# Performance work log

Measured on AMD Instinct MI355X. Metric: run time of the kernel, lower is better.

Reference implementation:

```python
import jax, jax.numpy as jnp
import numpy as np

S, B, E, H = 2048, 2, 1024, 16
D = E // H  # head_dim = 64


def setup_inputs() -> dict:
    key = jax.random.key(0)
    ks = jax.random.split(key, 11)
    std = 1.0 / np.sqrt(E)
    return {
        "query": jax.random.normal(ks[0], (S, B, E), jnp.float32),
        "key": jax.random.normal(ks[1], (S, B, E), jnp.float32),
        "value": jax.random.normal(ks[2], (S, B, E), jnp.float32),
        "q_w": jax.random.uniform(ks[3], (E, E), jnp.float32, -std, std),
        "q_b": jax.random.uniform(ks[4], (E,), jnp.float32, -std, std),
        "k_w": jax.random.uniform(ks[5], (E, E), jnp.float32, -std, std),
        "k_b": jax.random.uniform(ks[6], (E,), jnp.float32, -std, std),
        "v_w": jax.random.uniform(ks[7], (E, E), jnp.float32, -std, std),
        "v_b": jax.random.uniform(ks[8], (E,), jnp.float32, -std, std),
        "out_w": jax.random.uniform(ks[9], (E, E), jnp.float32, -std, std),
        "out_b": jax.random.uniform(ks[10], (E,), jnp.float32, -std, std),
    }


def reference(query, key, value, q_w, q_b, k_w, k_b, v_w, v_b, out_w, out_b):
    tgt_len, bsz, embed_dim = query.shape
    src_len = key.shape[0]
    head_dim = embed_dim // H
    scaling = head_dim ** -0.5

    # nn.Linear: x @ W.T + b
    q = (jnp.einsum('sbe,fe->sbf', query, q_w) + q_b) * scaling
    k = jnp.einsum('sbe,fe->sbf', key, k_w) + k_b
    v = jnp.einsum('sbe,fe->sbf', value, v_w) + v_b

    # [S, B, E] -> [B*H, S, D]
    def split_heads(x, n):
        return x.reshape(n, bsz * H, head_dim).transpose(1, 0, 2)

    q = split_heads(q, tgt_len)
    k = split_heads(k, src_len)
    v = split_heads(v, src_len)

    scores = jnp.einsum('bqd,bkd->bqk', q, k)        # [B*H, S, S]
    attn = jax.nn.softmax(scores, axis=-1)            # dropout p=0 -> identity
    out = jnp.einsum('bqk,bkd->bqd', attn, v)         # [B*H, S, D]
    out = out.transpose(1, 0, 2).reshape(tgt_len, bsz, embed_dim)
    Z = jnp.einsum('sbe,fe->sbf', out, out_w) + out_b
    attn_avg = attn.reshape(bsz, H, tgt_len, src_len).sum(axis=1) / H
    return Z, attn_avg
```

## Files before the change

kernel.cpp:

```cpp
#include <hip/hip_runtime.h>
#include <hip/hip_fp16.h>
#include <cstdint>
#include <cstddef>

#define S_LEN 2048
#define BATCH 2
#define EMB   1024
#define NHEAD 16
#define HDIM  64

typedef short short8 __attribute__((ext_vector_type(8)));
typedef float f32x4  __attribute__((ext_vector_type(4)));

__device__ __forceinline__ unsigned short f2b(float f) {
    unsigned int u = __float_as_uint(f);
    u = (u + 0x7FFFu + ((u >> 16) & 1u)) >> 16;
    return (unsigned short)u;
}
__device__ __forceinline__ unsigned int pk2(float a, float b) {
    return (unsigned int)f2b(a) | ((unsigned int)f2b(b) << 16);
}
__device__ __forceinline__ float b2f_lo(unsigned int u) { return __uint_as_float(u << 16); }
__device__ __forceinline__ float b2f_hi(unsigned int u) { return __uint_as_float(u & 0xFFFF0000u); }

__device__ __forceinline__ void gload_lds16(const ushort* g, ushort* l) {
    __builtin_amdgcn_global_load_lds(
        (const __attribute__((address_space(1))) void*)g,
        (__attribute__((address_space(3))) void*)l, 16, 0, 0);
}

__global__ __launch_bounds__(256)
void cast3(const float* __restrict__ s0, const float* __restrict__ s1,
           const float* __restrict__ s2, ushort* __restrict__ d0,
           ushort* __restrict__ d1, ushort* __restrict__ d2)
{
    const float* s = (blockIdx.y == 0) ? s0 : (blockIdx.y == 1) ? s1 : s2;
    ushort*      d = (blockIdx.y == 0) ? d0 : (blockIdx.y == 1) ? d1 : d2;
    const size_t i = ((size_t)blockIdx.x * 256 + threadIdx.x) * 8;
    const float4 a = *(const float4*)(s + i);
    const float4 b = *(const float4*)(s + i + 4);
    *(uint4*)(d + i) = make_uint4(pk2(a.x, a.y), pk2(a.z, a.w),
                                  pk2(b.x, b.y), pk2(b.z, b.w));
}

__global__ __launch_bounds__(256)
void cast4(const float* __restrict__ s0, const float* __restrict__ s1,
           const float* __restrict__ s2, const float* __restrict__ s3,
           ushort* __restrict__ d0, ushort* __restrict__ d1,
           ushort* __restrict__ d2, ushort* __restrict__ d3)
{
    const float* s = (blockIdx.y == 0) ? s0 : (blockIdx.y == 1) ? s1
                   : (blockIdx.y == 2) ? s2 : s3;
    ushort*      d = (blockIdx.y == 0) ? d0 : (blockIdx.y == 1) ? d1
                   : (blockIdx.y == 2) ? d2 : d3;
    const size_t i = ((size_t)blockIdx.x * 256 + threadIdx.x) * 8;
    const float4 a = *(const float4*)(s + i);
    const float4 b = *(const float4*)(s + i + 4);
    *(uint4*)(d + i) = make_uint4(pk2(a.x, a.y), pk2(a.z, a.w),
                                  pk2(b.x, b.y), pk2(b.z, b.w));
}

__device__ __forceinline__ void gemm_core(
    ushort (*As)[128 * 32], ushort (*Bs)[128 * 32],
    const ushort* __restrict__ A, const ushort* __restrict__ W,
    const float* __restrict__ bias, void* __restrict__ out_,
    float scale, int mode)
{
    constexpr int K  = EMB;
    constexpr int NT = K / 32;

    const int t    = threadIdx.x;
    const int lane = t & 63;
    const int wave = t >> 6;
    const int quad = lane >> 4;
    const int l15  = lane & 15;
    const int wm   = wave >> 2;
    const int wn   = wave & 3;
    const int m0   = blockIdx.x * 128;
    const int n0   = blockIdx.y * 128;

    const int srow = t >> 2;
    const int sseg = ((t & 3) ^ ((srow >> 1) & 3)) << 3;
    const ushort* gA = A + (size_t)(m0 + srow) * K + sseg;
    const ushort* gW = W + (size_t)(n0 + srow) * K + sseg;

    f32x4 acc[4][2];
#pragma unroll
    for (int mi = 0; mi < 4; ++mi)
#pragma unroll
        for (int ni = 0; ni < 2; ++ni) acc[mi][ni] = (f32x4){0.f, 0.f, 0.f, 0.f};

#define STAGE(buf, kt) do {                         \
        gload_lds16(gA + (kt) * 32, &As[buf][t * 8]); \
        gload_lds16(gW + (kt) * 32, &Bs[buf][t * 8]); \
    } while (0)

    STAGE(0, 0);
    __syncthreads();

    for (int kt = 0; kt < NT; ++kt) {
        const int cur = kt & 1;
        if (kt + 1 < NT) STAGE(cur ^ 1, kt + 1);
        short8 af[4], bf[2];
#pragma unroll
        for (int mi = 0; mi < 4; ++mi) {
            const int ra = wm * 64 + mi * 16 + l15;
            af[mi] = *(const short8*)&As[cur][ra * 32 + ((quad ^ ((ra >> 1) & 3)) << 3)];
        }
#pragma unroll
        for (int ni = 0; ni < 2; ++ni) {
            const int rb = wn * 32 + ni * 16 + l15;
            bf[ni] = *(const short8*)&Bs[cur][rb * 32 + ((quad ^ ((rb >> 1) & 3)) << 3)];
        }
#pragma unroll
        for (int mi = 0; mi < 4; ++mi)
#pragma unroll
            for (int ni = 0; ni < 2; ++ni)
                acc[mi][ni] = __builtin_amdgcn_mfma_f32_16x16x32_bf16(
                    af[mi], bf[ni], acc[mi][ni], 0, 0, 0);
        __syncthreads();
    }
#undef STAGE

#pragma unroll
    for (int mi = 0; mi < 4; ++mi)
#pragma unroll
        for (int ni = 0; ni < 2; ++ni) {
            const int col = n0 + wn * 32 + ni * 16 + l15;
            const float bc = bias[col];
#pragma unroll
            for (int r = 0; r < 4; ++r) {
                const int rg = m0 + wm * 64 + mi * 16 + quad * 4 + r;
                const float v = (acc[mi][ni][r] + bc) * scale;
                if (mode == 0) {
                    ((float*)out_)[(size_t)rg * EMB + col] = v;
                } else {
                    const int s  = rg >> 1;
                    const int bb = rg & 1;
                    const int h  = col >> 6;
                    const int d  = col & 63;
                    if (mode == 1)
                        ((ushort*)out_)[(((size_t)(bb * NHEAD + h)) * S_LEN + s) * HDIM + d] = f2b(v);
                    else
                        ((ushort*)out_)[(((size_t)(bb * NHEAD + h)) * HDIM + d) * S_LEN + s] = f2b(v);
                }
            }
        }
}

__global__ __launch_bounds__(512, 2)
void gemm_qkv(const ushort* __restrict__ qi, const ushort* __restrict__ ki,
              const ushort* __restrict__ vi,
              const ushort* __restrict__ qW, const ushort* __restrict__ kW,
              const ushort* __restrict__ vW,
              const float* __restrict__ qB, const float* __restrict__ kB,
              const float* __restrict__ vB,
              ushort* __restrict__ qO, ushort* __restrict__ kO,
              ushort* __restrict__ vO)
{
    __shared__ ushort As[2][128 * 32];
    __shared__ ushort Bs[2][128 * 32];
    const int z = blockIdx.z;
    const ushort* A    = (z == 0) ? qi : (z == 1) ? ki : vi;
    const ushort* W    = (z == 0) ? qW : (z == 1) ? kW : vW;
    const float* bias  = (z == 0) ? qB : (z == 1) ? kB : vB;
    ushort* out        = (z == 0) ? qO : (z == 1) ? kO : vO;
    const float scale  = (z == 0) ? 0.125f : 1.0f;
    const int   mode   = (z == 2) ? 2 : 1;
    gemm_core(As, Bs, A, W, bias, out, scale, mode);
}

__global__ __launch_bounds__(512, 2)
void gemm_z(const ushort* __restrict__ A, const ushort* __restrict__ W,
            const float* __restrict__ bias, float* __restrict__ out)
{
    __shared__ ushort As[2][128 * 32];
    __shared__ ushort Bs[2][128 * 32];
    gemm_core(As, Bs, A, W, bias, out, 1.0f, 0);
}

#define PLD 2056
__global__ __launch_bounds__(512, 4)
void attn_bf16(const ushort* __restrict__ qw, const ushort* __restrict__ kw,
               const ushort* __restrict__ vt, ushort* __restrict__ ao,
               float* __restrict__ rinv_ws)
{
    __shared__ ushort pLds[16 * PLD];
    __shared__ float  redS[8 * 16];
    __shared__ float  red2[4 * 16 * 16];

    const int t     = threadIdx.x;
    const int lane  = t & 63;
    const int wave  = t >> 6;
    const int quad  = lane >> 4;
    const int l15   = lane & 15;
    const int rbase = quad * 4;

    const int bid     = blockIdx.x;
    const int logical = (bid & 7) * 64 + (bid >> 3);
    const int qt      = logical & 127;
    const int rest    = logical >> 7;
    const int b       = rest & 1;
    const int g       = rest >> 1;
    const int sq0     = qt * 16;

    const int ntile = wave & 3;
    const int khalf = wave >> 2;

    for (int hh = 0; hh < 8; ++hh) {
        const int h  = g * 8 + hh;
        const int bh = b * NHEAD + h;
        const ushort* qbase = qw + ((size_t)bh * S_LEN + sq0) * HDIM;
        const ushort* kbse  = kw + (size_t)bh * S_LEN * HDIM;

        const short8 qf0 = *(const short8*)(qbase + l15 * HDIM + quad * 8);
        const short8 qf1 = *(const short8*)(qbase + l15 * HDIM + 32 + quad * 8);

        float s4[4] = {0.f, 0.f, 0.f, 0.f};
#pragma unroll
        for (int ti = 0; ti < 16; ++ti) {
            const int c0 = wave * 256 + ti * 16;
            const ushort* kr = kbse + (size_t)(c0 + l15) * HDIM;
            const short8 k0 = *(const short8*)(kr + quad * 8);
            const short8 k1 = *(const short8*)(kr + 32 + quad * 8);
            f32x4 a = (f32x4){0.f, 0.f, 0.f, 0.f};
            a = __builtin_amdgcn_mfma_f32_16x16x32_bf16(qf0, k0, a, 0, 0, 0);
            a = __builtin_amdgcn_mfma_f32_16x16x32_bf16(qf1, k1, a, 0, 0, 0);
#pragma unroll
            for (int r = 0; r < 4; ++r) {
                const float e = exp2f(fmaf(a[r], 1.44269504f, -11.54156035f));
                s4[r] += e;
                pLds[(rbase + r) * PLD + c0 + l15] = f2b(e);
            }
        }
#pragma unroll
        for (int off = 1; off < 16; off <<= 1)
#pragma unroll
            for (int r = 0; r < 4; ++r) s4[r] += __shfl_xor(s4[r], off, 16);
        if (l15 == 0)
#pragma unroll
            for (int r = 0; r < 4; ++r) redS[wave * 16 + rbase + r] = s4[r];
        __syncthreads();

        float rinv[4];
#pragma unroll
        for (int r = 0; r < 4; ++r) {
            float s = redS[rbase + r];
#pragma unroll
            for (int w = 1; w < 8; ++w) s += redS[w * 16 + rbase + r];
            rinv[r] = 1.0f / s;
        }
        if (wave == 0 && l15 == 0) {
#pragma unroll
            for (int r = 0; r < 4; ++r)
                rinv_ws[(size_t)bh * S_LEN + sq0 + rbase + r] = rinv[r];
        }

        const ushort* vrow = vt + ((size_t)bh * HDIM + ntile * 16 + l15) * S_LEN + khalf * 1024;
        const ushort* prow = &pLds[l15 * PLD + khalf * 1024];
        f32x4 o0 = (f32x4){0.f, 0.f, 0.f, 0.f}, o1 = o0;
#pragma unroll
        for (int st = 0; st < 32; st += 2) {
            const short8 pa0 = *(const short8*)(prow + st * 32 + quad * 8);
            const short8 vb0 = *(const short8*)(vrow + st * 32 + quad * 8);
            o0 = __builtin_amdgcn_mfma_f32_16x16x32_bf16(pa0, vb0, o0, 0, 0, 0);
            const short8 pa1 = *(const short8*)(prow + (st + 1) * 32 + quad * 8);
            const short8 vb1 = *(const short8*)(vrow + (st + 1) * 32 + quad * 8);
            o1 = __builtin_amdgcn_mfma_f32_16x16x32_bf16(pa1, vb1, o1, 0, 0, 0);
        }
        const f32x4 o = o0 + o1;
        if (khalf == 1) {
#pragma unroll
            for (int r = 0; r < 4; ++r)
                red2[ntile * 256 + (rbase + r) * 16 + l15] = o[r];
        }
        __syncthreads();
        if (khalf == 0) {
#pragma unroll
            for (int r = 0; r < 4; ++r) {
                const float val = (o[r] + red2[ntile * 256 + (rbase + r) * 16 + l15]) * rinv[r];
                const int s = sq0 + rbase + r;
                const int d = ntile * 16 + l15;
                ao[((size_t)s * BATCH + b) * EMB + h * HDIM + d] = f2b(val);
            }
        }
    }
}

__global__ __launch_bounds__(512, 2)
void pavg_scores(const ushort* __restrict__ qw, const ushort* __restrict__ kw,
                 const float* __restrict__ rinv_ws, float* __restrict__ out)
{
    const int t     = threadIdx.x;
    const int lane  = t & 63;
    const int wave  = t >> 6;
    const int quad  = lane >> 4;
    const int l15   = lane & 15;
    const int rbase = quad * 4;

    const int bid     = blockIdx.x;
    const int logical = (bid & 7) * 64 + (bid >> 3);
    const int kc      = logical >> 6;
    const int b       = (logical >> 5) & 1;
    const int sqc     = logical & 31;

    const int k0row = kc * 256 + wave * 32;

    float pacc[4][2][4];
#pragma unroll
    for (int s4i = 0; s4i < 4; ++s4i)
#pragma unroll
        for (int t2 = 0; t2 < 2; ++t2)
#pragma unroll
            for (int r = 0; r < 4; ++r) pacc[s4i][t2][r] = 0.f;

    for (int h = 0; h < NHEAD; ++h) {
        const int bh = b * NHEAD + h;
        const ushort* kr0 = kw + ((size_t)bh * S_LEN + k0row + l15) * HDIM;
        const ushort* kr1 = kw + ((size_t)bh * S_LEN + k0row + 16 + l15) * HDIM;
        const short8 kf00 = *(const short8*)(kr0 + quad * 8);
        const short8 kf01 = *(const short8*)(kr0 + 32 + quad * 8);
        const short8 kf10 = *(const short8*)(kr1 + quad * 8);
        const short8 kf11 = *(const short8*)(kr1 + 32 + quad * 8);
        const float* rbse = rinv_ws + (size_t)bh * S_LEN + sqc * 64;
#pragma unroll
        for (int s4i = 0; s4i < 4; ++s4i) {
            const ushort* qbase = qw + ((size_t)bh * S_LEN + sqc * 64 + s4i * 16) * HDIM;
            const short8 qf0 = *(const short8*)(qbase + l15 * HDIM + quad * 8);
            const short8 qf1 = *(const short8*)(qbase + l15 * HDIM + 32 + quad * 8);
            f32x4 a0 = (f32x4){0.f, 0.f, 0.f, 0.f}, a1 = a0;
            a0 = __builtin_amdgcn_mfma_f32_16x16x32_bf16(qf0, kf00, a0, 0, 0, 0);
            a0 = __builtin_amdgcn_mfma_f32_16x16x32_bf16(qf1, kf01, a0, 0, 0, 0);
            a1 = __builtin_amdgcn_mfma_f32_16x16x32_bf16(qf0, kf10, a1, 0, 0, 0);
            a1 = __builtin_amdgcn_mfma_f32_16x16x32_bf16(qf1, kf11, a1, 0, 0, 0);
#pragma unroll
            for (int r = 0; r < 4; ++r) {
                const float ri = rbse[s4i * 16 + rbase + r];
                pacc[s4i][0][r] = fmaf(exp2f(fmaf(a0[r], 1.44269504f, -11.54156035f)), ri, pacc[s4i][0][r]);
                pacc[s4i][1][r] = fmaf(exp2f(fmaf(a1[r], 1.44269504f, -11.54156035f)), ri, pacc[s4i][1][r]);
            }
        }
    }

    const float inv16 = 0.0625f;
#pragma unroll
    for (int s4i = 0; s4i < 4; ++s4i)
#pragma unroll
        for (int t2 = 0; t2 < 2; ++t2)
#pragma unroll
            for (int r = 0; r < 4; ++r) {
                const int sq = sqc * 64 + s4i * 16 + rbase + r;
                const int sk = k0row + t2 * 16 + l15;
                out[((size_t)b * S_LEN + sq) * S_LEN + sk] = pacc[s4i][t2][r] * inv16;
            }
}

extern "C" void kernel_launch(void* const* d_in, const int* in_sizes, int n_in,
                              void* d_out, int out_size, void* d_ws, size_t ws_size,
                              hipStream_t stream)
{
    const float* query = (const float*)d_in[0];
    const float* key   = (const float*)d_in[1];
    const float* value = (const float*)d_in[2];
    const float* q_w   = (const float*)d_in[3];
    const float* q_b   = (const float*)d_in[4];
    const float* k_w   = (const float*)d_in[5];
    const float* k_b   = (const float*)d_in[6];
    const float* v_w   = (const float*)d_in[7];
    const float* v_b   = (const float*)d_in[8];
    const float* out_w = (const float*)d_in[9];
    const float* out_b = (const float*)d_in[10];

    float* Z        = (float*)d_out;
    float* attn_avg = Z + (size_t)S_LEN * BATCH * EMB;

    const size_t QKV = (size_t)S_LEN * BATCH * EMB;
    ushort* q_ws    = (ushort*)d_ws;
    ushort* k_ws    = q_ws + QKV;
    ushort* vt_ws   = k_ws + QKV;
    ushort* ao_ws   = vt_ws + QKV;
    float*  rinv_ws = (float*)(ao_ws + QKV);
    ushort* qbf     = (ushort*)(rinv_ws + (size_t)BATCH * NHEAD * S_LEN);
    ushort* kbf     = qbf + QKV;
    ushort* vbf     = kbf + QKV;
    ushort* wqb     = vbf + QKV;
    ushort* wkb     = wqb + (size_t)EMB * EMB;
    ushort* wvb     = wkb + (size_t)EMB * EMB;
    ushort* wob     = wvb + (size_t)EMB * EMB;

    cast3<<<dim3(2048, 3), 256, 0, stream>>>(query, key, value, qbf, kbf, vbf);
    cast4<<<dim3(512, 4), 256, 0, stream>>>(q_w, k_w, v_w, out_w, wqb, wkb, wvb, wob);

    const dim3 blkG(512);
    const dim3 gq(32, 8, 3);
    gemm_qkv<<<gq, blkG, 0, stream>>>(qbf, kbf, vbf, wqb, wkb, wvb,
                                      q_b, k_b, v_b, q_ws, k_ws, vt_ws);

    attn_bf16<<<dim3(512), dim3(512), 0, stream>>>(q_ws, k_ws, vt_ws, ao_ws, rinv_ws);

    const dim3 gz(32, 8);
    gemm_z<<<gz, blkG, 0, stream>>>(ao_ws, wob, out_b, Z);

    pavg_scores<<<dim3(512), dim3(512), 0, stream>>>(q_ws, k_ws, rinv_ws, attn_avg);
}
```

Before: 518.1 us.

## Double-buffer K tiles in LDS and cache row inverses in pavg_scores

The head-averaged score kernel now stages each head's 256x64 K tile into LDS through async global-to-LDS loads, using an XOR swizzle and two buffers so the load for the next head overlaps compute on the current one. It also preloads all 16 heads' softmax row inverses for the block's 64 query rows into shared memory once. This replaces per-wave direct global K fragment loads and repeated global reads of the inverses. In exchange it uses about 68 KB of LDS per block and adds a barrier per head, which may cut occupancy against the launch bound of 2 blocks.

```diff
diff --git a/kernel.cpp b/kernel.cpp
--- a/kernel.cpp
+++ b/kernel.cpp
@@ -291,6 +291,9 @@
 void pavg_scores(const ushort* __restrict__ qw, const ushort* __restrict__ kw,
                  const float* __restrict__ rinv_ws, float* __restrict__ out)
 {
+    __shared__ ushort Kb[2][256 * 64];
+    __shared__ float  rl[16 * 64];
+
     const int t     = threadIdx.x;
     const int lane  = t & 63;
     const int wave  = t >> 6;
@@ -303,8 +306,25 @@
     const int kc      = logical >> 6;
     const int b       = (logical >> 5) & 1;
     const int sqc     = logical & 31;
-
-    const int k0row = kc * 256 + wave * 32;
+    const int k0row   = kc * 256;
+
+    {
+        int j = t;
+        rl[j] = rinv_ws[((size_t)b * NHEAD + (j >> 6)) * S_LEN + sqc * 64 + (j & 63)];
+        j = t + 512;
+        rl[j] = rinv_ws[((size_t)b * NHEAD + (j >> 6)) * S_LEN + sqc * 64 + (j & 63)];
+    }
+
+#define STAGEK(buf, h) do {                                                    \
+        const ushort* kg = kw + ((size_t)(b * NHEAD + (h)) * S_LEN + k0row) * HDIM; \
+        _Pragma("unroll")                                                      \
+        for (int i = 0; i < 4; ++i) {                                          \
+            const int idx = i * 512 + t;                                       \
+            const int rr  = idx >> 3;                                          \
+            const int ss  = (idx & 7) ^ (rr & 7);                              \
+            gload_lds16(kg + rr * HDIM + ss * 8, &Kb[buf][idx * 8]);           \
+        }                                                                      \
+    } while (0)
 
     float pacc[4][2][4];
 #pragma unroll
@@ -314,15 +334,21 @@
 #pragma unroll
             for (int r = 0; r < 4; ++r) pacc[s4i][t2][r] = 0.f;
 
+    STAGEK(0, 0);
+    __syncthreads();
+
     for (int h = 0; h < NHEAD; ++h) {
+        const int cur = h & 1;
+        if (h + 1 < NHEAD) STAGEK(cur ^ 1, h + 1);
+
+        const int r0 = wave * 32 + l15;
+        const int r1 = r0 + 16;
+        const short8 kf00 = *(const short8*)&Kb[cur][r0 * 64 + ((quad       ^ (r0 & 7)) << 3)];
+        const short8 kf01 = *(const short8*)&Kb[cur][r0 * 64 + (((quad + 4) ^ (r0 & 7)) << 3)];
+        const short8 kf10 = *(const short8*)&Kb[cur][r1 * 64 + ((quad       ^ (r1 & 7)) << 3)];
+        const short8 kf11 = *(const short8*)&Kb[cur][r1 * 64 + (((quad + 4) ^ (r1 & 7)) << 3)];
+
         const int bh = b * NHEAD + h;
-        const ushort* kr0 = kw + ((size_t)bh * S_LEN + k0row + l15) * HDIM;
-        const ushort* kr1 = kw + ((size_t)bh * S_LEN + k0row + 16 + l15) * HDIM;
-        const short8 kf00 = *(const short8*)(kr0 + quad * 8);
-        const short8 kf01 = *(const short8*)(kr0 + 32 + quad * 8);
-        const short8 kf10 = *(const short8*)(kr1 + quad * 8);
-        const short8 kf11 = *(const short8*)(kr1 + 32 + quad * 8);
-        const float* rbse = rinv_ws + (size_t)bh * S_LEN + sqc * 64;
 #pragma unroll
         for (int s4i = 0; s4i < 4; ++s4i) {
             const ushort* qbase = qw + ((size_t)bh * S_LEN + sqc * 64 + s4i * 16) * HDIM;
@@ -335,12 +361,14 @@
             a1 = __builtin_amdgcn_mfma_f32_16x16x32_bf16(qf1, kf11, a1, 0, 0, 0);
 #pragma unroll
             for (int r = 0; r < 4; ++r) {
-                const float ri = rbse[s4i * 16 + rbase + r];
+                const float ri = rl[h * 64 + s4i * 16 + rbase + r];
                 pacc[s4i][0][r] = fmaf(exp2f(fmaf(a0[r], 1.44269504f, -11.54156035f)), ri, pacc[s4i][0][r]);
                 pacc[s4i][1][r] = fmaf(exp2f(fmaf(a1[r], 1.44269504f, -11.54156035f)), ri, pacc[s4i][1][r]);
             }
         }
+        __syncthreads();
     }
+#undef STAGEK
 
     const float inv16 = 0.0625f;
 #pragma unroll
@@ -350,7 +378,7 @@
 #pragma unroll
             for (int r = 0; r < 4; ++r) {
                 const int sq = sqc * 64 + s4i * 16 + rbase + r;
-                const int sk = k0row + t2 * 16 + l15;
+                const int sk = k0row + wave * 32 + t2 * 16 + l15;
                 out[((size_t)b * S_LEN + sq) * S_LEN + sk] = pacc[s4i][t2][r] * inv16;
             }
 }
```

Result: faster. 492.0 us (-5.0%).
